# Optimization experiments

Hardware: AMD Instinct MI355X
Metric: run time of the kernel (lower is better)

The kernel has to match this reference:

```python
import jax, jax.numpy as jnp
import numpy as np

B, N, D_FEAT = 4, 2048, 3
P = B * N
C_KP, K_PTS, NSAMPLE = 64, 15, 64
RADIUS, WINDOW = 0.2, 0.25
KP_EXTENT = 0.08  # prev_grid_size * sigma
F, H, HID, L = 256, 8, 512, 2
DH = F // H
EPS = 1e-5


def setup_inputs() -> dict:
    key = jax.random.key(0)
    k = jax.random.split(key, 24)
    s = 0.02
    position = jax.random.uniform(k[0], (B, N, 3), jnp.float32)
    feature = jax.random.normal(k[1], (B, N, D_FEAT), jnp.float32)
    # KPConv kernel points: fixed points inside a ball of radius 1.5*KP_EXTENT
    d = jax.random.normal(k[2], (K_PTS, 3))
    d = d / jnp.clip(jnp.linalg.norm(d, axis=1, keepdims=True), 1e-6)
    r = jax.random.uniform(k[3], (K_PTS, 1)) ** (1.0 / 3.0)
    kernel_points = (d * r * 1.5 * KP_EXTENT).astype(jnp.float32)
    return dict(
        position=position,
        feature=feature,
        kernel_points=kernel_points,
        kp_weights=s * jax.random.normal(k[4], (K_PTS, D_FEAT, C_KP), jnp.float32),
        bn_gamma=jnp.ones((C_KP,), jnp.float32),
        bn_beta=jnp.zeros((C_KP,), jnp.float32),
        weightmatrix=jax.random.normal(k[5], (1, C_KP + 3, F), jnp.float32) * s,
        Wq=s * jax.random.normal(k[6], (L, F, F), jnp.float32),
        bq=jnp.zeros((L, F), jnp.float32),
        Wk=s * jax.random.normal(k[7], (L, F, F), jnp.float32),
        bk=jnp.zeros((L, F), jnp.float32),
        Wv=s * jax.random.normal(k[8], (L, F, F), jnp.float32),
        bv=jnp.zeros((L, F), jnp.float32),
        Wo=s * jax.random.normal(k[9], (L, F, F), jnp.float32),
        bo=jnp.zeros((L, F), jnp.float32),
        ln1_g=jnp.ones((L, F), jnp.float32),
        ln1_b=jnp.zeros((L, F), jnp.float32),
        W1=s * jax.random.normal(k[10], (L, F, HID), jnp.float32),
        b1=jnp.zeros((L, HID), jnp.float32),
        W2=s * jax.random.normal(k[11], (L, HID, F), jnp.float32),
        b2=jnp.zeros((L, F), jnp.float32),
        ln2_g=jnp.ones((L, F), jnp.float32),
        ln2_b=jnp.zeros((L, F), jnp.float32),
    )


def _ball_query(position):
    """partial_dense ball query: first NSAMPLE in-radius neighbors per point, fill=P."""
    def one(b, pb):
        d2 = jnp.sum((pb[:, None, :] - pb[None, :, :]) ** 2, -1)      # [N,N]
        within = d2 <= RADIUS ** 2
        # stable argsort puts in-radius indices first, in ascending index order
        order = jnp.argsort(jnp.where(within, 0, 1).astype(jnp.int32), axis=1)[:, :NSAMPLE]
        valid = jnp.arange(NSAMPLE)[None, :] < jnp.sum(within, axis=1)[:, None]
        return jnp.where(valid, order + b * N, P)
    return jax.vmap(one)(jnp.arange(B), position).reshape(P, NSAMPLE)


def _kpconv(pos_flat, feat_flat, idx, kernel_points, kp_weights, bn_gamma, bn_beta):
    pos_pad = jnp.concatenate([pos_flat, jnp.full((1, 3), 1e6, pos_flat.dtype)], 0)
    feat_pad = jnp.concatenate([feat_flat, jnp.zeros((1, feat_flat.shape[1]), feat_flat.dtype)], 0)
    neigh = pos_pad[idx] - pos_flat[:, None, :]                     # [P,NS,3]
    diff = neigh[:, :, None, :] - kernel_points[None, None]         # [P,NS,K,3]
    dist = jnp.sqrt(jnp.sum(diff * diff, -1) + 1e-12)               # [P,NS,K]
    infl = jnp.clip(1.0 - dist / KP_EXTENT, 0.0)                    # linear influence
    nf = feat_pad[idx]                                              # [P,NS,Din]
    wf = jnp.einsum('pnk,pnd->pkd', infl, nf)
    out = jnp.einsum('pkd,kdc->pc', wf, kp_weights)                 # [P,C]
    mu = out.mean(0)
    var = out.var(0)
    out = bn_gamma * (out - mu) * jax.lax.rsqrt(var + EPS) + bn_beta
    return jnp.where(out >= 0, out, 0.2 * out)                      # LeakyReLU(0.2)


def _cluster_mask(position):
    """grid_sample: same-voxel points attend to each other. Returns bool [B,N,N]."""
    start = position.min(axis=1, keepdims=True)
    cell = jnp.floor((position - start) / WINDOW).astype(jnp.int32)
    cid = cell[..., 0] * 4096 + cell[..., 1] * 64 + cell[..., 2]
    return cid[:, :, None] == cid[:, None, :]


def _ln(x, g, b):
    mu = x.mean(-1, keepdims=True)
    v = x.var(-1, keepdims=True)
    return g * (x - mu) * jax.lax.rsqrt(v + EPS) + b


def _enc(x, mask, Wq, bq, Wk, bk, Wv, bv, Wo, bo, g1, be1, W1, bb1, W2, bb2, g2, be2):
    q = (x @ Wq + bq).reshape(B, N, H, DH)
    k = (x @ Wk + bk).reshape(B, N, H, DH)
    v = (x @ Wv + bv).reshape(B, N, H, DH)
    s = jnp.einsum('bihd,bjhd->bhij', q, k) * (1.0 / np.sqrt(DH))
    s = jnp.where(mask[:, None, :, :], s, -1e9)
    p = jax.nn.softmax(s, -1)
    o = jnp.einsum('bhij,bjhd->bihd', p, v).reshape(B, N, F)
    x = _ln(x + o @ Wo + bo, g1, be1)
    h = jax.nn.relu(x @ W1 + bb1) @ W2 + bb2
    return _ln(x + h, g2, be2)


def reference(position, feature, kernel_points, kp_weights, bn_gamma, bn_beta, weightmatrix,
              Wq, bq, Wk, bk, Wv, bv, Wo, bo, ln1_g, ln1_b, W1, b1, W2, b2, ln2_g, ln2_b):
    pos_flat = position.reshape(P, 3)
    feat_flat = feature.reshape(P, D_FEAT)
    idx = _ball_query(position)
    kpf = _kpconv(pos_flat, feat_flat, idx, kernel_points, kp_weights, bn_gamma, bn_beta)
    kpf = kpf.reshape(B, N, C_KP)
    mask = _cluster_mask(position)
    pw = jnp.concatenate([position, kpf], -1)                       # [B,N,C+3]
    emb = jnp.einsum('bnc,cf->bnf', pw, weightmatrix[0])
    for l in range(L):
        emb = _enc(emb, mask, Wq[l], bq[l], Wk[l], bk[l], Wv[l], bv[l], Wo[l], bo[l],
                   ln1_g[l], ln1_b[l], W1[l], b1[l], W2[l], b2[l], ln2_g[l], ln2_b[l])
    return emb
```

## Files before the change

### kernel.cpp

```cpp
#include <hip/hip_runtime.h>
#include <math.h>

#define BATCH 4
#define NPTS  2048
#define PTS   8192
#define NS    64
#define KPTS  15
#define CKP   64
#define FDIM  256
#define HIDD  512
#define NHEAD 8
#define DHEAD 32
#define NLAY  2
#define R2    0.04f
#define KPE   0.08f
#define WIN   0.25f
#define EPSF  1e-5f
#define SCALE 0.17677669529663687f
#define CPITCH 264

typedef __attribute__((ext_vector_type(8))) short          short8;
typedef __attribute__((ext_vector_type(8))) unsigned short ushort8;
typedef __attribute__((ext_vector_type(4))) float          f32x4;

static __device__ __forceinline__ unsigned short f2bf(float f) {
    unsigned int u = __float_as_uint(f);
    unsigned int r = u + 0x7fffu + ((u >> 16) & 1u);
    return (unsigned short)(r >> 16);
}
static __device__ __forceinline__ float b2f(unsigned short u) {
    return __uint_as_float(((unsigned int)u) << 16);
}

__global__ __launch_bounds__(256) void prep_k(
    const float* __restrict__ pos,
    const float* __restrict__ Wq, const float* __restrict__ Wk,
    const float* __restrict__ Wv, const float* __restrict__ Wo,
    const float* __restrict__ W1, const float* __restrict__ W2,
    const float* __restrict__ bq, const float* __restrict__ bk,
    const float* __restrict__ bv,
    unsigned short* __restrict__ wT, float* __restrict__ bqkv,
    int* __restrict__ sorted, int* __restrict__ inv,
    int* __restrict__ offs, int* __restrict__ hist,
    unsigned long long* __restrict__ masks)
{
    __shared__ __align__(16) unsigned char sm[38400];
    int bid = blockIdx.x, tid = threadIdx.x;

    if (bid < 3072) {
        int z = bid >> 8, r = bid & 255;
        int bx = r & 15, by = r >> 4;
        int t = z >> 1, l = z & 1;
        const float* src; unsigned short* dst; int K, N;
        switch (t) {
            case 0: src=Wq+(size_t)l*65536;  dst=wT+(size_t)l*196608;           K=256; N=256; break;
            case 1: src=Wk+(size_t)l*65536;  dst=wT+(size_t)l*196608+65536;     K=256; N=256; break;
            case 2: src=Wv+(size_t)l*65536;  dst=wT+(size_t)l*196608+131072;    K=256; N=256; break;
            case 3: src=Wo+(size_t)l*65536;  dst=wT+393216+(size_t)l*65536;     K=256; N=256; break;
            case 4: src=W1+(size_t)l*131072; dst=wT+524288+(size_t)l*131072;    K=256; N=512; break;
            default:src=W2+(size_t)l*131072; dst=wT+786432+(size_t)l*131072;    K=512; N=256; break;
        }
        int n0 = bx*32, k0 = by*32;
        if (n0 >= N || k0 >= K) return;
        float* ld = (float*)sm;
        #pragma unroll
        for (int i = 0; i < 4; ++i) { int v=tid+i*256; int ty=v>>5, tx=v&31;
            ld[ty*33+tx] = src[(size_t)(k0+ty)*N + n0+tx]; }
        __syncthreads();
        #pragma unroll
        for (int i = 0; i < 4; ++i) { int v=tid+i*256; int ny=v>>5, nk=v&31;
            dst[(size_t)(n0+ny)*K + k0+nk] = f2bf(ld[nk*33+ny]); }
    } else if (bid < 3584) {
        int m_ = bid - 3072;
        int chunk = m_ & 31, b = (m_ >> 5) & 3, qg = m_ >> 7;
        int w = tid >> 6, lane = tid & 63;
        float* qx = (float*)sm; float* qy = qx + 512; float* qz = qy + 512;
        int qbase = qg * 512;
        for (int t = tid; t < 512; t += 256) {
            const float* q = pos + (size_t)(b*NPTS + qbase + t)*3;
            qx[t] = q[0]; qy[t] = q[1]; qz[t] = q[2];
        }
        const float* c = pos + (size_t)(b*NPTS + chunk*64 + lane)*3;
        float cx = c[0], cy = c[1], cz = c[2];
        __syncthreads();
        int q0 = w * 128;
        for (int i = 0; i < 128; ++i) {
            int qi = q0 + i;
            float dx = cx - qx[qi], dy = cy - qy[qi], dz = cz - qz[qi];
            float d2 = dx*dx + dy*dy + dz*dz;
            unsigned long long m = __ballot(d2 <= R2);
            if (lane == 0) masks[(size_t)(b*NPTS + qbase + qi)*32 + chunk] = m;
        }
    } else if (bid < 3588) {
        int b = bid - 3584;
        float* sx = (float*)sm; float* sy = sx + 256; float* sz = sy + 256;
        unsigned char* cid_s = sm + 3072;
        unsigned int* maskc = (unsigned int*)(sm + 5120);
        int* wpfx = (int*)(sm + 21504);
        int* tot  = (int*)(sm + 37888);
        int* off_c= (int*)(sm + 38144);
        float mx=1e30f, my=1e30f, mz=1e30f;
        for (int n = tid; n < NPTS; n += 256) {
            const float* q = pos + ((size_t)b*NPTS + n)*3;
            mx = fminf(mx, q[0]); my = fminf(my, q[1]); mz = fminf(mz, q[2]);
        }
        sx[tid]=mx; sy[tid]=my; sz[tid]=mz; __syncthreads();
        for (int o=128;o;o>>=1){ if(tid<o){sx[tid]=fminf(sx[tid],sx[tid+o]);sy[tid]=fminf(sy[tid],sy[tid+o]);sz[tid]=fminf(sz[tid],sz[tid+o]);} __syncthreads(); }
        float X = sx[0], Y = sy[0], Z = sz[0];
        __syncthreads();
        for (int i = tid; i < 64*64; i += 256) maskc[i] = 0u;
        __syncthreads();
        for (int n = tid; n < NPTS; n += 256) {
            const float* q = pos + ((size_t)b*NPTS + n)*3;
            int cx = (int)floorf((q[0]-X)/WIN);
            int cy = (int)floorf((q[1]-Y)/WIN);
            int cz = (int)floorf((q[2]-Z)/WIN);
            int c = (cx<<4) | (cy<<2) | cz;
            cid_s[n] = (unsigned char)c;
            atomicOr(&maskc[c*64 + (n>>5)], 1u << (n & 31));
        }
        __syncthreads();
        if (tid < 64) {
            int run = 0;
            for (int wd = 0; wd < 64; ++wd) { wpfx[tid*64+wd] = run; run += __popc(maskc[tid*64+wd]); }
            tot[tid] = run;
        }
        __syncthreads();
        if (tid == 0) { int run = 0; for (int c = 0; c < 64; ++c) { off_c[c] = run; run += tot[c]; } }
        __syncthreads();
        if (tid < 64) { hist[b*64+tid] = tot[tid]; offs[b*64+tid] = off_c[tid]; }
        for (int n = tid; n < NPTS; n += 256) {
            int c = cid_s[n];
            int wd = n >> 5;
            int rank = wpfx[c*64+wd] + __popc(maskc[c*64+wd] & ((1u << (n & 31)) - 1u));
            int slot = b*NPTS + off_c[c] + rank;
            int p = b*NPTS + n;
            sorted[slot] = p;
            inv[p] = slot;
        }
    } else {
        int i = (bid - 3588)*256 + tid;
        if (i < 2*768) {
            int l = i / 768, n = i - l*768;
            float v = (n < 256) ? bq[l*256+n] : (n < 512) ? bk[l*256+n-256] : bv[l*256+n-512];
            bqkv[l*768 + n] = v;
        }
    }
}

__global__ __launch_bounds__(256) void kpc_k(
    const float* __restrict__ pos, const float* __restrict__ feat,
    const unsigned long long* __restrict__ masks,
    const float* __restrict__ kpts, const float* __restrict__ kpw,
    float* __restrict__ raw)
{
    __shared__ int   idxs[64][66];
    __shared__ float kpwl[45*64];
    __shared__ float kpl[48];
    __shared__ float wfp[64*181 + 4];

    int tid = threadIdx.x, w = tid >> 6, lane = tid & 63;
    int pb = blockIdx.x * 64;
    int b = pb >> 11;
    int base = b * NPTS;

    for (int t = tid; t < 45*64; t += 256) kpwl[t] = kpw[t];
    if (tid < 45) kpl[tid] = kpts[tid];

    int g = tid >> 5, j = tid & 31;
    for (int pp = 0; pp < 8; ++pp) {
        int lp = pp*8 + g;
        unsigned long long m = masks[(size_t)(pb + lp)*32 + j];
        int cnt = __popcll(m);
        int inc = cnt;
        #pragma unroll
        for (int off = 1; off < 32; off <<= 1) {
            int v = __shfl_up(inc, off, 32);
            if (j >= off) inc += v;
        }
        int pfx = inc - cnt;
        int total = __shfl(inc, 31, 32);
        unsigned long long mm = m; int slot = pfx;
        while (mm && slot < NS) {
            int bit = __ffsll((long long)mm) - 1;
            idxs[lp][slot++] = j*64 + bit;
            mm &= mm - 1;
        }
        int cc = total < NS ? total : NS;
        for (int s = cc + j; s < NS; s += 32) idxs[lp][s] = NPTS;
    }
    __syncthreads();

    float wf[45];
    #pragma unroll
    for (int t = 0; t < 45; ++t) wf[t] = 0.f;
    {
        int p = pb + lane;
        float xi = pos[(size_t)p*3+0], yi = pos[(size_t)p*3+1], zi = pos[(size_t)p*3+2];
        for (int n = w*16; n < w*16 + 16; ++n) {
            int id = idxs[lane][n];
            if (id < NPTS) {
                const float* pq = pos + (size_t)(base + id)*3;
                float rx = pq[0]-xi, ry = pq[1]-yi, rz = pq[2]-zi;
                const float* ff = feat + (size_t)(base + id)*3;
                float g0 = ff[0], g1 = ff[1], g2 = ff[2];
                #pragma unroll
                for (int k = 0; k < KPTS; ++k) {
                    float dx = rx - kpl[k*3+0], dy = ry - kpl[k*3+1], dz = rz - kpl[k*3+2];
                    float dist = sqrtf(dx*dx + dy*dy + dz*dz + 1e-12f);
                    float infl = fmaxf(0.f, 1.0f - dist * (1.0f/KPE));
                    wf[k*3+0] = fmaf(infl, g0, wf[k*3+0]);
                    wf[k*3+1] = fmaf(infl, g1, wf[k*3+1]);
                    wf[k*3+2] = fmaf(infl, g2, wf[k*3+2]);
                }
            }
        }
    }
    #pragma unroll
    for (int t = 0; t < 45; ++t) wfp[lane*181 + t*4 + w] = wf[t];
    __syncthreads();
    for (int i = tid; i < 64*45; i += 256) {
        int p_ = i / 45, t = i - p_*45;
        float* q = &wfp[p_*181 + t*4];
        q[0] = (q[0]+q[1]) + (q[2]+q[3]);
    }
    __syncthreads();
    {
        int c = tid & 63, pg = tid >> 6;
        float kw[45];
        #pragma unroll
        for (int t = 0; t < 45; ++t) kw[t] = kpwl[t*64 + c];
        for (int p0 = 0; p0 < 16; p0 += 4) {
            float a0=0.f, a1=0.f, a2=0.f, a3=0.f;
            int pl = pg*16 + p0;
            #pragma unroll
            for (int t = 0; t < 45; ++t) {
                a0 = fmaf(kw[t], wfp[(pl+0)*181 + t*4], a0);
                a1 = fmaf(kw[t], wfp[(pl+1)*181 + t*4], a1);
                a2 = fmaf(kw[t], wfp[(pl+2)*181 + t*4], a2);
                a3 = fmaf(kw[t], wfp[(pl+3)*181 + t*4], a3);
            }
            raw[(size_t)(pb + pl+0)*CKP + c] = a0;
            raw[(size_t)(pb + pl+1)*CKP + c] = a1;
            raw[(size_t)(pb + pl+2)*CKP + c] = a2;
            raw[(size_t)(pb + pl+3)*CKP + c] = a3;
        }
    }
}

__global__ void bn_stats_k(const float* __restrict__ raw, float* __restrict__ stats)
{
    int c = blockIdx.x, tid = threadIdx.x;
    float s = 0.f, q = 0.f;
    for (int p = tid; p < PTS; p += 256) { float v = raw[p*CKP + c]; s += v; q += v*v; }
    __shared__ float sh[256], sh2[256];
    sh[tid]=s; sh2[tid]=q; __syncthreads();
    for (int o = 128; o; o >>= 1) { if (tid < o) { sh[tid]+=sh[tid+o]; sh2[tid]+=sh2[tid+o]; } __syncthreads(); }
    if (tid == 0) { stats[c] = sh[0]; stats[CKP + c] = sh2[0]; }
}

__global__ void embed_k(const float* __restrict__ pos, const float* __restrict__ raw,
                        const float* __restrict__ stats, const float* __restrict__ gamma,
                        const float* __restrict__ beta, const float* __restrict__ Wm,
                        const int* __restrict__ inv,
                        float* __restrict__ xs, unsigned short* __restrict__ xsb)
{
    int p = blockIdx.x, tid = threadIdx.x;
    __shared__ float pw[67];
    if (tid < 3) pw[tid] = pos[p*3 + tid];
    else if (tid < 67) {
        int c = tid - 3;
        float mu  = stats[c] * (1.0f/PTS);
        float var = stats[CKP+c] * (1.0f/PTS) - mu*mu;
        float v = raw[p*CKP + c];
        float h = gamma[c] * (v - mu) * rsqrtf(var + EPSF) + beta[c];
        pw[tid] = h >= 0.f ? h : 0.2f * h;
    }
    __syncthreads();
    float acc = 0.f;
    for (int c = 0; c < 67; ++c) acc += pw[c] * Wm[c*FDIM + tid];
    int slot = inv[p];
    xs[(size_t)slot*FDIM + tid] = acc;
    xsb[(size_t)slot*FDIM + tid] = f2bf(acc);
}

template<int ACT, int MR>
__global__ __launch_bounds__(256) void bgemm256_k(
    const unsigned short* __restrict__ A, const unsigned short* __restrict__ Wt,
    const float* __restrict__ bias,
    unsigned short* __restrict__ Cb,
    int Nc, int K)
{
    __shared__ unsigned short As[MR*16*72];
    __shared__ unsigned short Bs[256*72];
    int tid = threadIdx.x;
    int l = tid & 63, wc = tid >> 6;
    int lr = l & 15, lk = l >> 4;
    int bm = blockIdx.y * (MR*16), bn = blockIdx.x * 256;

    f32x4 acc[MR][4] = {};

    for (int k0 = 0; k0 < K; k0 += 64) {
        __syncthreads();
        #pragma unroll
        for (int i = 0; i < MR/2; ++i) {
            int id = tid + i*256;
            int row = id >> 3, seg = id & 7;
            *(ushort8*)&As[row*72 + seg*8] =
                *(const ushort8*)&A[(size_t)(bm + row)*K + k0 + seg*8];
        }
        #pragma unroll
        for (int i = 0; i < 8; ++i) {
            int id = tid + i*256;
            int row = id >> 3, seg = id & 7;
            *(ushort8*)&Bs[row*72 + seg*8] =
                *(const ushort8*)&Wt[(size_t)(bn + row)*K + k0 + seg*8];
        }
        __syncthreads();
        #pragma unroll
        for (int kk = 0; kk < 64; kk += 32) {
            short8 b[4];
            #pragma unroll
            for (int ni = 0; ni < 4; ++ni)
                b[ni] = *(const short8*)&Bs[(wc*64 + ni*16 + lr)*72 + kk + lk*8];
            #pragma unroll
            for (int mi = 0; mi < MR; ++mi) {
                short8 a = *(const short8*)&As[(mi*16 + lr)*72 + kk + lk*8];
                #pragma unroll
                for (int ni = 0; ni < 4; ++ni)
                    acc[mi][ni] = __builtin_amdgcn_mfma_f32_16x16x32_bf16(
                        a, b[ni], acc[mi][ni], 0, 0, 0);
            }
        }
    }

    #pragma unroll
    for (int mi = 0; mi < MR; ++mi) {
        #pragma unroll
        for (int r = 0; r < 4; ++r) {
            int row = bm + mi*16 + lk*4 + r;
            #pragma unroll
            for (int ni = 0; ni < 4; ++ni) {
                int col = bn + wc*64 + ni*16 + lr;
                float v = acc[mi][ni][r] + bias[col];
                if (ACT == 1) v = v > 0.f ? v : 0.f;
                Cb[(size_t)row*Nc + col] = f2bf(v);
            }
        }
    }
}

__global__ __launch_bounds__(512) void attn2_k(
    const unsigned short* __restrict__ qkv, const unsigned short* __restrict__ WoT,
    const float* __restrict__ bo, const float* __restrict__ xs,
    const float* __restrict__ g, const float* __restrict__ be,
    const int* __restrict__ offs, const int* __restrict__ hist,
    float* __restrict__ x2, unsigned short* __restrict__ x2b)
{
    int cci = blockIdx.x, b = blockIdx.y;
    int Mc = hist[b*64 + cci];
    if (Mc == 0) return;
    int off = b*NPTS + offs[b*64 + cci];

    __shared__ unsigned short Kl[64*CPITCH];
    __shared__ unsigned short Vl[64*CPITCH];
    __shared__ unsigned short Pl[8][64*72];

    unsigned short* Ol = Kl;
    unsigned short* Bs = &Pl[0][0];
    float* red_s = (float*)Vl;
    float* red_q = red_s + 512;

    int tid = threadIdx.x;
    int w = tid >> 6, l = tid & 63;
    int lr = l & 15, lk = l >> 4;

    for (int r0 = 0; r0 < Mc; r0 += 64) {
        int nr = (Mc - r0) < 64 ? (Mc - r0) : 64;

        if (Mc <= 64) {
            #pragma unroll
            for (int it = 0; it < 4; ++it) {
                int id = tid + it*512;
                int key = id >> 5, ch8 = (id & 31)*8;
                ushort8 kv, vv;
                if (key < Mc) {
                    kv = *(const ushort8*)&qkv[(size_t)(off+key)*768 + 256 + ch8];
                    vv = *(const ushort8*)&qkv[(size_t)(off+key)*768 + 512 + ch8];
                } else {
                    kv = (ushort8)0; vv = (ushort8)0;
                }
                *(ushort8*)&Kl[key*CPITCH + ch8] = kv;
                *(ushort8*)&Vl[key*CPITCH + ch8] = vv;
            }
            __syncthreads();

            int h = w;
            f32x4 s[4][4] = {};
            short8 a[4], bb[4];
            #pragma unroll
            for (int mi = 0; mi < 4; ++mi) {
                int rg = off + mi*16 + lr;
                if (rg > PTS-1) rg = PTS-1;
                a[mi] = *(const short8*)&qkv[(size_t)rg*768 + h*32 + lk*8];
            }
            #pragma unroll
            for (int ni = 0; ni < 4; ++ni)
                bb[ni] = *(const short8*)&Kl[(ni*16+lr)*CPITCH + h*32 + lk*8];
            #pragma unroll
            for (int mi = 0; mi < 4; ++mi)
                #pragma unroll
                for (int ni = 0; ni < 4; ++ni)
                    s[mi][ni] = __builtin_amdgcn_mfma_f32_16x16x32_bf16(a[mi], bb[ni], s[mi][ni], 0, 0, 0);

            unsigned short* Pw = Pl[w];
            float invl[4][4];
            #pragma unroll
            for (int mi = 0; mi < 4; ++mi) {
                #pragma unroll
                for (int r = 0; r < 4; ++r) {
                    int row = mi*16 + lk*4 + r;
                    float sv[4]; float mx = -1e30f;
                    #pragma unroll
                    for (int ni = 0; ni < 4; ++ni) {
                        int col = ni*16 + lr;
                        float x = s[mi][ni][r] * SCALE;
                        sv[ni] = (col < Mc) ? x : -1e30f;
                        mx = fmaxf(mx, sv[ni]);
                    }
                    mx = fmaxf(mx, __shfl_xor(mx, 1));
                    mx = fmaxf(mx, __shfl_xor(mx, 2));
                    mx = fmaxf(mx, __shfl_xor(mx, 4));
                    mx = fmaxf(mx, __shfl_xor(mx, 8));
                    float ls = 0.f;
                    #pragma unroll
                    for (int ni = 0; ni < 4; ++ni) {
                        float e = __expf(sv[ni] - mx);
                        ls += e;
                        Pw[row*72 + ni*16 + lr] = f2bf(e);
                    }
                    ls += __shfl_xor(ls, 1);
                    ls += __shfl_xor(ls, 2);
                    ls += __shfl_xor(ls, 4);
                    ls += __shfl_xor(ls, 8);
                    invl[mi][r] = 1.0f / ls;
                }
            }

            f32x4 oacc[4][2] = {};
            #pragma unroll
            for (int ks = 0; ks < 2; ++ks) {
                short8 bv[2];
                #pragma unroll
                for (int db = 0; db < 2; ++db) {
                    short8 t;
                    #pragma unroll
                    for (int e = 0; e < 8; ++e)
                        t[e] = (short)Vl[(ks*32 + lk*8 + e)*CPITCH + h*32 + db*16 + lr];
                    bv[db] = t;
                }
                #pragma unroll
                for (int mi = 0; mi < 4; ++mi) {
                    short8 pa = *(const short8*)&Pw[(mi*16+lr)*72 + ks*32 + lk*8];
                    #pragma unroll
                    for (int db = 0; db < 2; ++db)
                        oacc[mi][db] = __builtin_amdgcn_mfma_f32_16x16x32_bf16(pa, bv[db], oacc[mi][db], 0, 0, 0);
                }
            }
            __syncthreads();
            #pragma unroll
            for (int mi = 0; mi < 4; ++mi)
                #pragma unroll
                for (int db = 0; db < 2; ++db)
                    #pragma unroll
                    for (int r = 0; r < 4; ++r) {
                        int row = mi*16 + lk*4 + r;
                        Ol[row*CPITCH + h*32 + db*16 + lr] =
                            f2bf(oacc[mi][db][r] * invl[mi][r]);
                    }
        } else {
            __syncthreads();
            for (int task = tid; task < nr*NHEAD; task += 512) {
                int row = task >> 3, h = task & 7;
                float qr[DHEAD];
                #pragma unroll
                for (int d = 0; d < DHEAD; ++d)
                    qr[d] = b2f(qkv[(size_t)(off+r0+row)*768 + h*32 + d]);
                float m = -3e38f, lsum = 0.f, acc[DHEAD];
                #pragma unroll
                for (int d = 0; d < DHEAD; ++d) acc[d] = 0.f;
                for (int jj = 0; jj < Mc; ++jj) {
                    float dot = 0.f;
                    #pragma unroll
                    for (int d = 0; d < DHEAD; ++d)
                        dot += qr[d] * b2f(qkv[(size_t)(off+jj)*768 + 256 + h*32 + d]);
                    float sc = dot * SCALE;
                    float mn = fmaxf(m, sc);
                    float aa = __expf(m - mn);
                    float e  = __expf(sc - mn);
                    lsum = lsum*aa + e;
                    #pragma unroll
                    for (int d = 0; d < DHEAD; ++d)
                        acc[d] = acc[d]*aa + e * b2f(qkv[(size_t)(off+jj)*768 + 512 + h*32 + d]);
                    m = mn;
                }
                float inv = 1.0f / lsum;
                #pragma unroll
                for (int d = 0; d < DHEAD; ++d)
                    Ol[row*CPITCH + h*32 + d] = f2bf(acc[d]*inv);
            }
        }
        __syncthreads();

        f32x4 acc2[4][2] = {};
        for (int k0 = 0; k0 < 256; k0 += 64) {
            #pragma unroll
            for (int i = 0; i < 4; ++i) {
                int id = tid + i*512;
                int rown = id >> 3, seg = id & 7;
                *(ushort8*)&Bs[rown*72 + seg*8] =
                    *(const ushort8*)&WoT[(size_t)rown*FDIM + k0 + seg*8];
            }
            __syncthreads();
            #pragma unroll
            for (int kk = 0; kk < 64; kk += 32) {
                short8 a2[4], b2r[2];
                #pragma unroll
                for (int mi = 0; mi < 4; ++mi)
                    a2[mi] = *(const short8*)&Ol[(mi*16+lr)*CPITCH + k0 + kk + lk*8];
                #pragma unroll
                for (int ni = 0; ni < 2; ++ni)
                    b2r[ni] = *(const short8*)&Bs[(w*32 + ni*16 + lr)*72 + kk + lk*8];
                #pragma unroll
                for (int mi = 0; mi < 4; ++mi)
                    #pragma unroll
                    for (int ni = 0; ni < 2; ++ni)
                        acc2[mi][ni] = __builtin_amdgcn_mfma_f32_16x16x32_bf16(
                            a2[mi], b2r[ni], acc2[mi][ni], 0, 0, 0);
            }
            __syncthreads();
        }

        #pragma unroll
        for (int mi = 0; mi < 4; ++mi) {
            #pragma unroll
            for (int r = 0; r < 4; ++r) {
                int row = mi*16 + lk*4 + r;
                int srow = off + r0 + row;
                if (srow > PTS-1) srow = PTS-1;
                #pragma unroll
                for (int ni = 0; ni < 2; ++ni) {
                    int col = w*32 + ni*16 + lr;
                    acc2[mi][ni][r] += bo[col] + xs[(size_t)srow*FDIM + col];
                }
            }
        }
        #pragma unroll
        for (int mi = 0; mi < 4; ++mi) {
            #pragma unroll
            for (int r = 0; r < 4; ++r) {
                float ps = 0.f, pq = 0.f;
                #pragma unroll
                for (int ni = 0; ni < 2; ++ni) { float v = acc2[mi][ni][r]; ps += v; pq += v*v; }
                ps += __shfl_xor(ps, 1);  pq += __shfl_xor(pq, 1);
                ps += __shfl_xor(ps, 2);  pq += __shfl_xor(pq, 2);
                ps += __shfl_xor(ps, 4);  pq += __shfl_xor(pq, 4);
                ps += __shfl_xor(ps, 8);  pq += __shfl_xor(pq, 8);
                if (lr == 0) {
                    int row = mi*16 + lk*4 + r;
                    red_s[w*64 + row] = ps;
                    red_q[w*64 + row] = pq;
                }
            }
        }
        __syncthreads();
        #pragma unroll
        for (int mi = 0; mi < 4; ++mi) {
            #pragma unroll
            for (int r = 0; r < 4; ++r) {
                int row = mi*16 + lk*4 + r;
                float s = 0.f, q = 0.f;
                #pragma unroll
                for (int ww = 0; ww < 8; ++ww) { s += red_s[ww*64 + row]; q += red_q[ww*64 + row]; }
                float mu  = s * (1.0f/FDIM);
                float var = q * (1.0f/FDIM) - mu*mu;
                float rs  = rsqrtf(var + EPSF);
                if (row < nr) {
                    int srow = off + r0 + row;
                    #pragma unroll
                    for (int ni = 0; ni < 2; ++ni) {
                        int col = w*32 + ni*16 + lr;
                        float o = g[col]*(acc2[mi][ni][r]-mu)*rs + be[col];
                        x2[(size_t)srow*FDIM + col] = o;
                        x2b[(size_t)srow*FDIM + col] = f2bf(o);
                    }
                }
            }
        }
        __syncthreads();
    }
}

template<int FINAL>
__global__ __launch_bounds__(256) void ffn_k(
    const unsigned short* __restrict__ A,
    const unsigned short* __restrict__ W1T,
    const float* __restrict__ b1,
    const unsigned short* __restrict__ W2T,
    const float* __restrict__ b2,
    const float* __restrict__ R,
    const float* __restrict__ g, const float* __restrict__ be,
    const int* __restrict__ sorted,
    float* __restrict__ Cf, unsigned short* __restrict__ Cb)
{
    __shared__ unsigned short As[32*264];
    __shared__ unsigned short Bs1[64*264];
    __shared__ unsigned short Bs2[256*72];
    __shared__ unsigned short Hs[32*72];
    __shared__ float red_s[4][32], red_q[4][32];

    int tid = threadIdx.x;
    int l = tid & 63, wc = tid >> 6;
    int lr = l & 15, lk = l >> 4;
    int bm = blockIdx.x * 32;

    #pragma unroll
    for (int i = 0; i < 4; ++i) {
        int id = tid + i*256;
        int row = id >> 5, seg = id & 31;
        *(ushort8*)&As[row*264 + seg*8] =
            *(const ushort8*)&A[(size_t)(bm + row)*FDIM + seg*8];
    }

    f32x4 acc[2][4] = {};

    for (int hc = 0; hc < 8; ++hc) {
        __syncthreads();
        #pragma unroll
        for (int i = 0; i < 8; ++i) {
            int id = tid + i*256;
            int row = id >> 5, seg = id & 31;
            *(ushort8*)&Bs1[row*264 + seg*8] =
                *(const ushort8*)&W1T[(size_t)(hc*64 + row)*FDIM + seg*8];
        }
        #pragma unroll
        for (int i = 0; i < 8; ++i) {
            int id = tid + i*256;
            int row = id >> 3, seg = id & 7;
            *(ushort8*)&Bs2[row*72 + seg*8] =
                *(const ushort8*)&W2T[(size_t)row*HIDD + hc*64 + seg*8];
        }
        __syncthreads();

        f32x4 h[2] = {};
        #pragma unroll
        for (int kk = 0; kk < 256; kk += 32) {
            short8 bfr = *(const short8*)&Bs1[(wc*16 + lr)*264 + kk + lk*8];
            #pragma unroll
            for (int mi = 0; mi < 2; ++mi) {
                short8 a = *(const short8*)&As[(mi*16 + lr)*264 + kk + lk*8];
                h[mi] = __builtin_amdgcn_mfma_f32_16x16x32_bf16(a, bfr, h[mi], 0, 0, 0);
            }
        }
        #pragma unroll
        for (int mi = 0; mi < 2; ++mi)
            #pragma unroll
            for (int r = 0; r < 4; ++r) {
                int row = mi*16 + lk*4 + r;
                int hcol = wc*16 + lr;
                float v = h[mi][r] + b1[hc*64 + hcol];
                v = v > 0.f ? v : 0.f;
                Hs[row*72 + hcol] = f2bf(v);
            }
        __syncthreads();

        #pragma unroll
        for (int kk = 0; kk < 64; kk += 32) {
            short8 pa[2], wb[4];
            #pragma unroll
            for (int mi = 0; mi < 2; ++mi)
                pa[mi] = *(const short8*)&Hs[(mi*16 + lr)*72 + kk + lk*8];
            #pragma unroll
            for (int ni = 0; ni < 4; ++ni)
                wb[ni] = *(const short8*)&Bs2[(wc*64 + ni*16 + lr)*72 + kk + lk*8];
            #pragma unroll
            for (int mi = 0; mi < 2; ++mi)
                #pragma unroll
                for (int ni = 0; ni < 4; ++ni)
                    acc[mi][ni] = __builtin_amdgcn_mfma_f32_16x16x32_bf16(
                        pa[mi], wb[ni], acc[mi][ni], 0, 0, 0);
        }
    }

    #pragma unroll
    for (int mi = 0; mi < 2; ++mi) {
        #pragma unroll
        for (int r = 0; r < 4; ++r) {
            int row = bm + mi*16 + lk*4 + r;
            #pragma unroll
            for (int ni = 0; ni < 4; ++ni) {
                int col = wc*64 + ni*16 + lr;
                acc[mi][ni][r] += b2[col] + R[(size_t)row*FDIM + col];
            }
        }
    }
    #pragma unroll
    for (int mi = 0; mi < 2; ++mi) {
        #pragma unroll
        for (int r = 0; r < 4; ++r) {
            float ps = 0.f, pq = 0.f;
            #pragma unroll
            for (int ni = 0; ni < 4; ++ni) { float v = acc[mi][ni][r]; ps += v; pq += v*v; }
            ps += __shfl_xor(ps, 1);  pq += __shfl_xor(pq, 1);
            ps += __shfl_xor(ps, 2);  pq += __shfl_xor(pq, 2);
            ps += __shfl_xor(ps, 4);  pq += __shfl_xor(pq, 4);
            ps += __shfl_xor(ps, 8);  pq += __shfl_xor(pq, 8);
            if (lr == 0) {
                int rl = mi*16 + lk*4 + r;
                red_s[wc][rl] = ps;
                red_q[wc][rl] = pq;
            }
        }
    }
    __syncthreads();
    #pragma unroll
    for (int mi = 0; mi < 2; ++mi) {
        #pragma unroll
        for (int r = 0; r < 4; ++r) {
            int rl = mi*16 + lk*4 + r;
            float s = red_s[0][rl] + red_s[1][rl] + red_s[2][rl] + red_s[3][rl];
            float q = red_q[0][rl] + red_q[1][rl] + red_q[2][rl] + red_q[3][rl];
            float mu  = s * (1.0f/FDIM);
            float var = q * (1.0f/FDIM) - mu*mu;
            float rs  = rsqrtf(var + EPSF);
            int row = bm + rl;
            #pragma unroll
            for (int ni = 0; ni < 4; ++ni) {
                int col = wc*64 + ni*16 + lr;
                float o = g[col]*(acc[mi][ni][r]-mu)*rs + be[col];
                if (FINAL) Cf[(size_t)sorted[row]*FDIM + col] = o;
                else       Cf[(size_t)row*FDIM + col] = o;
                if (Cb) Cb[(size_t)row*FDIM + col] = f2bf(o);
            }
        }
    }
}

extern "C" void kernel_launch(void* const* d_in, const int* in_sizes, int n_in,
                              void* d_out, int out_size, void* d_ws, size_t ws_size,
                              hipStream_t stream)
{
    (void)in_sizes; (void)n_in; (void)out_size; (void)ws_size;
    const float* pos  = (const float*)d_in[0];
    const float* feat = (const float*)d_in[1];
    const float* kpts = (const float*)d_in[2];
    const float* kpw  = (const float*)d_in[3];
    const float* bn_g = (const float*)d_in[4];
    const float* bn_b = (const float*)d_in[5];
    const float* Wm   = (const float*)d_in[6];
    const float* Wq   = (const float*)d_in[7];
    const float* bq   = (const float*)d_in[8];
    const float* Wk   = (const float*)d_in[9];
    const float* bk   = (const float*)d_in[10];
    const float* Wv   = (const float*)d_in[11];
    const float* bv   = (const float*)d_in[12];
    const float* Wo   = (const float*)d_in[13];
    const float* bo   = (const float*)d_in[14];
    const float* g1   = (const float*)d_in[15];
    const float* be1  = (const float*)d_in[16];
    const float* W1   = (const float*)d_in[17];
    const float* bb1  = (const float*)d_in[18];
    const float* W2   = (const float*)d_in[19];
    const float* bb2  = (const float*)d_in[20];
    const float* g2   = (const float*)d_in[21];
    const float* be2  = (const float*)d_in[22];

    char* ws = (char*)d_ws;
    const size_t MB = 1024*1024;
    float* raw    = (float*)(ws + 0);
    unsigned long long* masks = (unsigned long long*)(ws + 2*MB);
    float* stats  = (float*)(ws + 4*MB);
    int*   hist   = (int*)(ws + 4*MB + 4096);
    int*   offs   = hist + 256;
    int*   sorted = (int*)(ws + 4*MB + 16384);
    int*   inv    = sorted + PTS;
    float* xs   = (float*)(ws + 5*MB);
    float* x2   = (float*)(ws + 13*MB);
    unsigned short* xsb   = (unsigned short*)(ws + 21*MB);
    unsigned short* x2b   = (unsigned short*)(ws + 25*MB);
    unsigned short* qkvb  = (unsigned short*)(ws + 29*MB);
    unsigned short* wT    = (unsigned short*)(ws + 45*MB);
    float*          bqkv  = (float*)(ws + 47*MB);

    prep_k<<<3594, 256, 0, stream>>>(pos, Wq, Wk, Wv, Wo, W1, W2, bq, bk, bv,
                                     wT, bqkv, sorted, inv, offs, hist, masks);
    kpc_k<<<PTS/64, 256, 0, stream>>>(pos, feat, masks, kpts, kpw, raw);
    bn_stats_k<<<CKP, 256, 0, stream>>>(raw, stats);
    embed_k<<<PTS, 256, 0, stream>>>(pos, raw, stats, bn_g, bn_b, Wm, inv, xs, xsb);

    for (int l = 0; l < NLAY; ++l) {
        const unsigned short* W1T_l = wT + 524288 + (size_t)l*131072;
        const unsigned short* W2T_l = wT + 786432 + (size_t)l*131072;
        bgemm256_k<0,8><<<dim3(3, PTS/128), 256, 0, stream>>>(
            xsb, wT + (size_t)l*196608, bqkv + l*768, qkvb, 768, FDIM);
        attn2_k<<<dim3(64, BATCH), 512, 0, stream>>>(
            qkvb, wT + 393216 + (size_t)l*65536, bo + l*FDIM, xs,
            g1 + l*FDIM, be1 + l*FDIM, offs, hist, x2, x2b);
        if (l == NLAY-1)
            ffn_k<1><<<PTS/32, 256, 0, stream>>>(
                x2b, W1T_l, bb1 + l*HIDD, W2T_l, bb2 + l*FDIM, x2,
                g2 + l*FDIM, be2 + l*FDIM, sorted, (float*)d_out, nullptr);
        else
            ffn_k<0><<<PTS/32, 256, 0, stream>>>(
                x2b, W1T_l, bb1 + l*HIDD, W2T_l, bb2 + l*FDIM, x2,
                g2 + l*FDIM, be2 + l*FDIM, nullptr, xs, xsb);
    }
}
```

Before: 215.2 us.

## Fuse per-layer QKV GEMM, attention and FFN into one cooperative persistent kernel

Replaces the three per-layer launches (QKV GEMM, attention+Wo+LN, FFN+LN) across two layers with a single cooperative kernel of 256 blocks that steps through the stages with grid-wide syncs. The aim is to remove launch overhead and inter-kernel gaps. In exchange the grid is limited to 256 blocks of 512 threads with about 138 KB of LDS each, which gives low occupancy for the GEMM and FFN phases. Grid syncs and thread fences also add cost.

```diff
diff --git a/kernel.cpp b/kernel.cpp
--- a/kernel.cpp
+++ b/kernel.cpp
@@ -1,5 +1,8 @@
 #include <hip/hip_runtime.h>
+#include <hip/hip_cooperative_groups.h>
 #include <math.h>
+
+namespace cg = cooperative_groups;
 
 #define BATCH 4
 #define NPTS  2048
@@ -284,466 +287,484 @@
     xsb[(size_t)slot*FDIM + tid] = f2bf(acc);
 }
 
-template<int ACT, int MR>
-__global__ __launch_bounds__(256) void bgemm256_k(
-    const unsigned short* __restrict__ A, const unsigned short* __restrict__ Wt,
-    const float* __restrict__ bias,
-    unsigned short* __restrict__ Cb,
-    int Nc, int K)
+__global__ __launch_bounds__(512) void mega_k(
+    const unsigned short* __restrict__ xsb_in, float* __restrict__ xs,
+    unsigned short* __restrict__ xsb,
+    const unsigned short* __restrict__ wT, const float* __restrict__ bqkv,
+    const float* __restrict__ bo, const float* __restrict__ g1,
+    const float* __restrict__ be1, const float* __restrict__ bb1,
+    const float* __restrict__ bb2, const float* __restrict__ g2,
+    const float* __restrict__ be2,
+    const int* __restrict__ offs, const int* __restrict__ hist,
+    const int* __restrict__ sorted,
+    unsigned short* __restrict__ qkvb, float* __restrict__ x2,
+    unsigned short* __restrict__ x2b, float* __restrict__ dout)
 {
-    __shared__ unsigned short As[MR*16*72];
-    __shared__ unsigned short Bs[256*72];
-    int tid = threadIdx.x;
-    int l = tid & 63, wc = tid >> 6;
-    int lr = l & 15, lk = l >> 4;
-    int bm = blockIdx.y * (MR*16), bn = blockIdx.x * 256;
-
-    f32x4 acc[MR][4] = {};
-
-    for (int k0 = 0; k0 < K; k0 += 64) {
-        __syncthreads();
-        #pragma unroll
-        for (int i = 0; i < MR/2; ++i) {
-            int id = tid + i*256;
-            int row = id >> 3, seg = id & 7;
-            *(ushort8*)&As[row*72 + seg*8] =
-                *(const ushort8*)&A[(size_t)(bm + row)*K + k0 + seg*8];
-        }
-        #pragma unroll
-        for (int i = 0; i < 8; ++i) {
-            int id = tid + i*256;
-            int row = id >> 3, seg = id & 7;
-            *(ushort8*)&Bs[row*72 + seg*8] =
-                *(const ushort8*)&Wt[(size_t)(bn + row)*K + k0 + seg*8];
-        }
-        __syncthreads();
-        #pragma unroll
-        for (int kk = 0; kk < 64; kk += 32) {
-            short8 b[4];
+    __shared__ __align__(16) unsigned char smem[141312];
+    cg::grid_group grid = cg::this_grid();
+
+    int bid = blockIdx.x, tid = threadIdx.x;
+    int w = tid >> 6, l_ = tid & 63;
+    int lr = l_ & 15, lk = l_ >> 4;
+
+    for (int l = 0; l < NLAY; ++l) {
+        const unsigned short* WqkvT = wT + (size_t)l*196608;
+        const unsigned short* WoT   = wT + 393216 + (size_t)l*65536;
+        const unsigned short* W1T   = wT + 524288 + (size_t)l*131072;
+        const unsigned short* W2T   = wT + 786432 + (size_t)l*131072;
+        const float* bqkv_l = bqkv + l*768;
+        const float* bo_l   = bo  + l*FDIM;
+        const float* g1_l   = g1  + l*FDIM;
+        const float* be1_l  = be1 + l*FDIM;
+        const float* b1_l   = bb1 + l*HIDD;
+        const float* b2_l   = bb2 + l*FDIM;
+        const float* g2_l   = g2  + l*FDIM;
+        const float* be2_l  = be2 + l*FDIM;
+
+        if (bid < 192) {
+            unsigned short* As = (unsigned short*)smem;
+            unsigned short* Bs = As + 128*72;
+            int bm = (bid / 3) * 128, bn = (bid % 3) * 256;
+            int wr = w >> 2, wc4 = w & 3;
+            f32x4 acc[4][4] = {};
+            for (int k0 = 0; k0 < FDIM; k0 += 64) {
+                __syncthreads();
+                #pragma unroll
+                for (int i = 0; i < 2; ++i) {
+                    int id = tid + i*512;
+                    int row = id >> 3, seg = id & 7;
+                    *(ushort8*)&As[row*72 + seg*8] =
+                        *(const ushort8*)&xsb[(size_t)(bm + row)*FDIM + k0 + seg*8];
+                }
+                #pragma unroll
+                for (int i = 0; i < 4; ++i) {
+                    int id = tid + i*512;
+                    int row = id >> 3, seg = id & 7;
+                    *(ushort8*)&Bs[row*72 + seg*8] =
+                        *(const ushort8*)&WqkvT[(size_t)(bn + row)*FDIM + k0 + seg*8];
+                }
+                __syncthreads();
+                #pragma unroll
+                for (int kk = 0; kk < 64; kk += 32) {
+                    short8 bb[4];
+                    #pragma unroll
+                    for (int ni = 0; ni < 4; ++ni)
+                        bb[ni] = *(const short8*)&Bs[(wc4*64 + ni*16 + lr)*72 + kk + lk*8];
+                    #pragma unroll
+                    for (int mi = 0; mi < 4; ++mi) {
+                        short8 a = *(const short8*)&As[(wr*64 + mi*16 + lr)*72 + kk + lk*8];
+                        #pragma unroll
+                        for (int ni = 0; ni < 4; ++ni)
+                            acc[mi][ni] = __builtin_amdgcn_mfma_f32_16x16x32_bf16(
+                                a, bb[ni], acc[mi][ni], 0, 0, 0);
+                    }
+                }
+            }
             #pragma unroll
-            for (int ni = 0; ni < 4; ++ni)
-                b[ni] = *(const short8*)&Bs[(wc*64 + ni*16 + lr)*72 + kk + lk*8];
+            for (int mi = 0; mi < 4; ++mi)
+                #pragma unroll
+                for (int r = 0; r < 4; ++r) {
+                    int row = bm + wr*64 + mi*16 + lk*4 + r;
+                    #pragma unroll
+                    for (int ni = 0; ni < 4; ++ni) {
+                        int col = bn + wc4*64 + ni*16 + lr;
+                        qkvb[(size_t)row*768 + col] = f2bf(acc[mi][ni][r] + bqkv_l[col]);
+                    }
+                }
+        }
+        __threadfence();
+        grid.sync();
+
+        {
+            int cci = bid & 63, bb_ = bid >> 6;
+            int Mc = hist[bb_*64 + cci];
+            if (Mc != 0) {
+                int off = bb_*NPTS + offs[bb_*64 + cci];
+                unsigned short* Kl = (unsigned short*)smem;
+                unsigned short* Vl = Kl + 64*CPITCH;
+                unsigned short* Pl = Vl + 64*CPITCH;
+                unsigned short* Ol = Kl;
+                unsigned short* Bs = Pl;
+                float* red_s = (float*)Vl;
+                float* red_q = red_s + 512;
+
+                for (int r0 = 0; r0 < Mc; r0 += 64) {
+                    int nr = (Mc - r0) < 64 ? (Mc - r0) : 64;
+
+                    if (Mc <= 64) {
+                        #pragma unroll
+                        for (int it = 0; it < 4; ++it) {
+                            int id = tid + it*512;
+                            int key = id >> 5, ch8 = (id & 31)*8;
+                            ushort8 kv, vv;
+                            if (key < Mc) {
+                                kv = *(const ushort8*)&qkvb[(size_t)(off+key)*768 + 256 + ch8];
+                                vv = *(const ushort8*)&qkvb[(size_t)(off+key)*768 + 512 + ch8];
+                            } else {
+                                kv = (ushort8)0; vv = (ushort8)0;
+                            }
+                            *(ushort8*)&Kl[key*CPITCH + ch8] = kv;
+                            *(ushort8*)&Vl[key*CPITCH + ch8] = vv;
+                        }
+                        __syncthreads();
+
+                        int h = w;
+                        f32x4 s[4][4] = {};
+                        short8 a[4], bb[4];
+                        #pragma unroll
+                        for (int mi = 0; mi < 4; ++mi) {
+                            int rg = off + mi*16 + lr;
+                            if (rg > PTS-1) rg = PTS-1;
+                            a[mi] = *(const short8*)&qkvb[(size_t)rg*768 + h*32 + lk*8];
+                        }
+                        #pragma unroll
+                        for (int ni = 0; ni < 4; ++ni)
+                            bb[ni] = *(const short8*)&Kl[(ni*16+lr)*CPITCH + h*32 + lk*8];
+                        #pragma unroll
+                        for (int mi = 0; mi < 4; ++mi)
+                            #pragma unroll
+                            for (int ni = 0; ni < 4; ++ni)
+                                s[mi][ni] = __builtin_amdgcn_mfma_f32_16x16x32_bf16(a[mi], bb[ni], s[mi][ni], 0, 0, 0);
+
+                        unsigned short* Pw = Pl + w*4608;
+                        float invl[4][4];
+                        #pragma unroll
+                        for (int mi = 0; mi < 4; ++mi) {
+                            #pragma unroll
+                            for (int r = 0; r < 4; ++r) {
+                                int row = mi*16 + lk*4 + r;
+                                float sv[4]; float mx = -1e30f;
+                                #pragma unroll
+                                for (int ni = 0; ni < 4; ++ni) {
+                                    int col = ni*16 + lr;
+                                    float x = s[mi][ni][r] * SCALE;
+                                    sv[ni] = (col < Mc) ? x : -1e30f;
+                                    mx = fmaxf(mx, sv[ni]);
+                                }
+                                mx = fmaxf(mx, __shfl_xor(mx, 1));
+                                mx = fmaxf(mx, __shfl_xor(mx, 2));
+                                mx = fmaxf(mx, __shfl_xor(mx, 4));
+                                mx = fmaxf(mx, __shfl_xor(mx, 8));
+                                float ls = 0.f;
+                                #pragma unroll
+                                for (int ni = 0; ni < 4; ++ni) {
+                                    float e = __expf(sv[ni] - mx);
+                                    ls += e;
+                                    Pw[row*72 + ni*16 + lr] = f2bf(e);
+                                }
+                                ls += __shfl_xor(ls, 1);
+                                ls += __shfl_xor(ls, 2);
+                                ls += __shfl_xor(ls, 4);
+                                ls += __shfl_xor(ls, 8);
+                                invl[mi][r] = 1.0f / ls;
+                            }
+                        }
+
+                        f32x4 oacc[4][2] = {};
+                        #pragma unroll
+                        for (int ks = 0; ks < 2; ++ks) {
+                            short8 bv[2];
+                            #pragma unroll
+                            for (int db = 0; db < 2; ++db) {
+                                short8 t;
+                                #pragma unroll
+                                for (int e = 0; e < 8; ++e)
+                                    t[e] = (short)Vl[(ks*32 + lk*8 + e)*CPITCH + h*32 + db*16 + lr];
+                                bv[db] = t;
+                            }
+                            #pragma unroll
+                            for (int mi = 0; mi < 4; ++mi) {
+                                short8 pa = *(const short8*)&Pw[(mi*16+lr)*72 + ks*32 + lk*8];
+                                #pragma unroll
+                                for (int db = 0; db < 2; ++db)
+                                    oacc[mi][db] = __builtin_amdgcn_mfma_f32_16x16x32_bf16(pa, bv[db], oacc[mi][db], 0, 0, 0);
+                            }
+                        }
+                        __syncthreads();
+                        #pragma unroll
+                        for (int mi = 0; mi < 4; ++mi)
+                            #pragma unroll
+                            for (int db = 0; db < 2; ++db)
+                                #pragma unroll
+                                for (int r = 0; r < 4; ++r) {
+                                    int row = mi*16 + lk*4 + r;
+                                    Ol[row*CPITCH + h*32 + db*16 + lr] =
+                                        f2bf(oacc[mi][db][r] * invl[mi][r]);
+                                }
+                    } else {
+                        __syncthreads();
+                        for (int task = tid; task < nr*NHEAD; task += 512) {
+                            int row = task >> 3, h = task & 7;
+                            float qr[DHEAD];
+                            #pragma unroll
+                            for (int d = 0; d < DHEAD; ++d)
+                                qr[d] = b2f(qkvb[(size_t)(off+r0+row)*768 + h*32 + d]);
+                            float m = -3e38f, lsum = 0.f, acc[DHEAD];
+                            #pragma unroll
+                            for (int d = 0; d < DHEAD; ++d) acc[d] = 0.f;
+                            for (int jj = 0; jj < Mc; ++jj) {
+                                float dot = 0.f;
+                                #pragma unroll
+                                for (int d = 0; d < DHEAD; ++d)
+                                    dot += qr[d] * b2f(qkvb[(size_t)(off+jj)*768 + 256 + h*32 + d]);
+                                float sc = dot * SCALE;
+                                float mn = fmaxf(m, sc);
+                                float aa = __expf(m - mn);
+                                float e  = __expf(sc - mn);
+                                lsum = lsum*aa + e;
+                                #pragma unroll
+                                for (int d = 0; d < DHEAD; ++d)
+                                    acc[d] = acc[d]*aa + e * b2f(qkvb[(size_t)(off+jj)*768 + 512 + h*32 + d]);
+                                m = mn;
+                            }
+                            float inv = 1.0f / lsum;
+                            #pragma unroll
+                            for (int d = 0; d < DHEAD; ++d)
+                                Ol[row*CPITCH + h*32 + d] = f2bf(acc[d]*inv);
+                        }
+                    }
+                    __syncthreads();
+
+                    f32x4 acc2[4][2] = {};
+                    for (int k0 = 0; k0 < 256; k0 += 64) {
+                        #pragma unroll
+                        for (int i = 0; i < 4; ++i) {
+                            int id = tid + i*512;
+                            int rown = id >> 3, seg = id & 7;
+                            *(ushort8*)&Bs[rown*72 + seg*8] =
+                                *(const ushort8*)&WoT[(size_t)rown*FDIM + k0 + seg*8];
+                        }
+                        __syncthreads();
+                        #pragma unroll
+                        for (int kk = 0; kk < 64; kk += 32) {
+                            short8 a2[4], b2r[2];
+                            #pragma unroll
+                            for (int mi = 0; mi < 4; ++mi)
+                                a2[mi] = *(const short8*)&Ol[(mi*16+lr)*CPITCH + k0 + kk + lk*8];
+                            #pragma unroll
+                            for (int ni = 0; ni < 2; ++ni)
+                                b2r[ni] = *(const short8*)&Bs[(w*32 + ni*16 + lr)*72 + kk + lk*8];
+                            #pragma unroll
+                            for (int mi = 0; mi < 4; ++mi)
+                                #pragma unroll
+                                for (int ni = 0; ni < 2; ++ni)
+                                    acc2[mi][ni] = __builtin_amdgcn_mfma_f32_16x16x32_bf16(
+                                        a2[mi], b2r[ni], acc2[mi][ni], 0, 0, 0);
+                        }
+                        __syncthreads();
+                    }
+
+                    #pragma unroll
+                    for (int mi = 0; mi < 4; ++mi) {
+                        #pragma unroll
+                        for (int r = 0; r < 4; ++r) {
+                            int row = mi*16 + lk*4 + r;
+                            int srow = off + r0 + row;
+                            if (srow > PTS-1) srow = PTS-1;
+                            #pragma unroll
+                            for (int ni = 0; ni < 2; ++ni) {
+                                int col = w*32 + ni*16 + lr;
+                                acc2[mi][ni][r] += bo_l[col] + xs[(size_t)srow*FDIM + col];
+                            }
+                        }
+                    }
+                    #pragma unroll
+                    for (int mi = 0; mi < 4; ++mi) {
+                        #pragma unroll
+                        for (int r = 0; r < 4; ++r) {
+                            float ps = 0.f, pq = 0.f;
+                            #pragma unroll
+                            for (int ni = 0; ni < 2; ++ni) { float v = acc2[mi][ni][r]; ps += v; pq += v*v; }
+                            ps += __shfl_xor(ps, 1);  pq += __shfl_xor(pq, 1);
+                            ps += __shfl_xor(ps, 2);  pq += __shfl_xor(pq, 2);
+                            ps += __shfl_xor(ps, 4);  pq += __shfl_xor(pq, 4);
+                            ps += __shfl_xor(ps, 8);  pq += __shfl_xor(pq, 8);
+                            if (lr == 0) {
+                                int row = mi*16 + lk*4 + r;
+                                red_s[w*64 + row] = ps;
+                                red_q[w*64 + row] = pq;
+                            }
+                        }
+                    }
+                    __syncthreads();
+                    #pragma unroll
+                    for (int mi = 0; mi < 4; ++mi) {
+                        #pragma unroll
+                        for (int r = 0; r < 4; ++r) {
+                            int row = mi*16 + lk*4 + r;
+                            float s_ = 0.f, q_ = 0.f;
+                            #pragma unroll
+                            for (int ww = 0; ww < 8; ++ww) { s_ += red_s[ww*64 + row]; q_ += red_q[ww*64 + row]; }
+                            float mu  = s_ * (1.0f/FDIM);
+                            float var = q_ * (1.0f/FDIM) - mu*mu;
+                            float rs  = rsqrtf(var + EPSF);
+                            if (row < nr) {
+                                int srow = off + r0 + row;
+                                #pragma unroll
+                                for (int ni = 0; ni < 2; ++ni) {
+                                    int col = w*32 + ni*16 + lr;
+                                    float o = g1_l[col]*(acc2[mi][ni][r]-mu)*rs + be1_l[col];
+                                    x2[(size_t)srow*FDIM + col] = o;
+                                    x2b[(size_t)srow*FDIM + col] = f2bf(o);
+                                }
+                            }
+                        }
+                    }
+                    __syncthreads();
+                }
+            }
+        }
+        __threadfence();
+        grid.sync();
+
+        {
+            unsigned short* As  = (unsigned short*)smem;
+            unsigned short* Bs1 = As + 32*264;
+            unsigned short* Bs2 = Bs1 + 64*264;
+            unsigned short* Hs  = Bs2 + 256*72;
+            float* red_s = (float*)(Hs + 32*72);
+            float* red_q = red_s + 128;
+            int bm = bid * 32;
+            int wc = w;
+
             #pragma unroll
-            for (int mi = 0; mi < MR; ++mi) {
-                short8 a = *(const short8*)&As[(mi*16 + lr)*72 + kk + lk*8];
-                #pragma unroll
-                for (int ni = 0; ni < 4; ++ni)
-                    acc[mi][ni] = __builtin_amdgcn_mfma_f32_16x16x32_bf16(
-                        a, b[ni], acc[mi][ni], 0, 0, 0);
+            for (int i = 0; i < 2; ++i) {
+                int id = tid + i*512;
+                int row = id >> 5, seg = id & 31;
+                *(ushort8*)&As[row*264 + seg*8] =
+                    *(const ushort8*)&x2b[(size_t)(bm + row)*FDIM + seg*8];
             }
-        }
-    }
-
-    #pragma unroll
-    for (int mi = 0; mi < MR; ++mi) {
-        #pragma unroll
-        for (int r = 0; r < 4; ++r) {
-            int row = bm + mi*16 + lk*4 + r;
-            #pragma unroll
-            for (int ni = 0; ni < 4; ++ni) {
-                int col = bn + wc*64 + ni*16 + lr;
-                float v = acc[mi][ni][r] + bias[col];
-                if (ACT == 1) v = v > 0.f ? v : 0.f;
-                Cb[(size_t)row*Nc + col] = f2bf(v);
+
+            f32x4 acc[2][4] = {};
+
+            for (int hc = 0; hc < 8; ++hc) {
+                __syncthreads();
+                #pragma unroll
+                for (int i = 0; i < 4; ++i) {
+                    int id = tid + i*512;
+                    int row = id >> 5, seg = id & 31;
+                    *(ushort8*)&Bs1[row*264 + seg*8] =
+                        *(const ushort8*)&W1T[(size_t)(hc*64 + row)*FDIM + seg*8];
+                }
+                #pragma unroll
+                for (int i = 0; i < 4; ++i) {
+                    int id = tid + i*512;
+                    int row = id >> 3, seg = id & 7;
+                    *(ushort8*)&Bs2[row*72 + seg*8] =
+                        *(const ushort8*)&W2T[(size_t)row*HIDD + hc*64 + seg*8];
+                }
+                __syncthreads();
+
+                if (tid < 256) {
+                    f32x4 h[2] = {};
+                    #pragma unroll
+                    for (int kk = 0; kk < 256; kk += 32) {
+                        short8 bfr = *(const short8*)&Bs1[(wc*16 + lr)*264 + kk + lk*8];
+                        #pragma unroll
+                        for (int mi = 0; mi < 2; ++mi) {
+                            short8 a = *(const short8*)&As[(mi*16 + lr)*264 + kk + lk*8];
+                            h[mi] = __builtin_amdgcn_mfma_f32_16x16x32_bf16(a, bfr, h[mi], 0, 0, 0);
+                        }
+                    }
+                    #pragma unroll
+                    for (int mi = 0; mi < 2; ++mi)
+                        #pragma unroll
+                        for (int r = 0; r < 4; ++r) {
+                            int row = mi*16 + lk*4 + r;
+                            int hcol = wc*16 + lr;
+                            float v = h[mi][r] + b1_l[hc*64 + hcol];
+                            v = v > 0.f ? v : 0.f;
+                            Hs[row*72 + hcol] = f2bf(v);
+                        }
+                }
+                __syncthreads();
+
+                if (tid < 256) {
+                    #pragma unroll
+                    for (int kk = 0; kk < 64; kk += 32) {
+                        short8 pa[2], wb[4];
+                        #pragma unroll
+                        for (int mi = 0; mi < 2; ++mi)
+                            pa[mi] = *(const short8*)&Hs[(mi*16 + lr)*72 + kk + lk*8];
+                        #pragma unroll
+                        for (int ni = 0; ni < 4; ++ni)
+                            wb[ni] = *(const short8*)&Bs2[(wc*64 + ni*16 + lr)*72 + kk + lk*8];
+                        #pragma unroll
+                        for (int mi = 0; mi < 2; ++mi)
+                            #pragma unroll
+                            for (int ni = 0; ni < 4; ++ni)
+                                acc[mi][ni] = __builtin_amdgcn_mfma_f32_16x16x32_bf16(
+                                    pa[mi], wb[ni], acc[mi][ni], 0, 0, 0);
+                    }
+                }
             }
-        }
-    }
-}
-
-__global__ __launch_bounds__(512) void attn2_k(
-    const unsigned short* __restrict__ qkv, const unsigned short* __restrict__ WoT,
-    const float* __restrict__ bo, const float* __restrict__ xs,
-    const float* __restrict__ g, const float* __restrict__ be,
-    const int* __restrict__ offs, const int* __restrict__ hist,
-    float* __restrict__ x2, unsigned short* __restrict__ x2b)
-{
-    int cci = blockIdx.x, b = blockIdx.y;
-    int Mc = hist[b*64 + cci];
-    if (Mc == 0) return;
-    int off = b*NPTS + offs[b*64 + cci];
-
-    __shared__ unsigned short Kl[64*CPITCH];
-    __shared__ unsigned short Vl[64*CPITCH];
-    __shared__ unsigned short Pl[8][64*72];
-
-    unsigned short* Ol = Kl;
-    unsigned short* Bs = &Pl[0][0];
-    float* red_s = (float*)Vl;
-    float* red_q = red_s + 512;
-
-    int tid = threadIdx.x;
-    int w = tid >> 6, l = tid & 63;
-    int lr = l & 15, lk = l >> 4;
-
-    for (int r0 = 0; r0 < Mc; r0 += 64) {
-        int nr = (Mc - r0) < 64 ? (Mc - r0) : 64;
-
-        if (Mc <= 64) {
-            #pragma unroll
-            for (int it = 0; it < 4; ++it) {
-                int id = tid + it*512;
-                int key = id >> 5, ch8 = (id & 31)*8;
-                ushort8 kv, vv;
-                if (key < Mc) {
-                    kv = *(const ushort8*)&qkv[(size_t)(off+key)*768 + 256 + ch8];
-                    vv = *(const ushort8*)&qkv[(size_t)(off+key)*768 + 512 + ch8];
-                } else {
-                    kv = (ushort8)0; vv = (ushort8)0;
-                }
-                *(ushort8*)&Kl[key*CPITCH + ch8] = kv;
-                *(ushort8*)&Vl[key*CPITCH + ch8] = vv;
+
+            if (tid < 256) {
+                #pragma unroll
+                for (int mi = 0; mi < 2; ++mi) {
+                    #pragma unroll
+                    for (int r = 0; r < 4; ++r) {
+                        int row = bm + mi*16 + lk*4 + r;
+                        #pragma unroll
+                        for (int ni = 0; ni < 4; ++ni) {
+                            int col = wc*64 + ni*16 + lr;
+                            acc[mi][ni][r] += b2_l[col] + x2[(size_t)row*FDIM + col];
+                        }
+                    }
+                }
+                #pragma unroll
+                for (int mi = 0; mi < 2; ++mi) {
+                    #pragma unroll
+                    for (int r = 0; r < 4; ++r) {
+                        float ps = 0.f, pq = 0.f;
+                        #pragma unroll
+                        for (int ni = 0; ni < 4; ++ni) { float v = acc[mi][ni][r]; ps += v; pq += v*v; }
+                        ps += __shfl_xor(ps, 1);  pq += __shfl_xor(pq, 1);
+                        ps += __shfl_xor(ps, 2);  pq += __shfl_xor(pq, 2);
+                        ps += __shfl_xor(ps, 4);  pq += __shfl_xor(pq, 4);
+                        ps += __shfl_xor(ps, 8);  pq += __shfl_xor(pq, 8);
+                        if (lr == 0) {
+                            int rl = mi*16 + lk*4 + r;
+                            red_s[wc*32 + rl] = ps;
+                            red_q[wc*32 + rl] = pq;
+                        }
+                    }
+                }
             }
             __syncthreads();
-
-            int h = w;
-            f32x4 s[4][4] = {};
-            short8 a[4], bb[4];
-            #pragma unroll
-            for (int mi = 0; mi < 4; ++mi) {
-                int rg = off + mi*16 + lr;
-                if (rg > PTS-1) rg = PTS-1;
-                a[mi] = *(const short8*)&qkv[(size_t)rg*768 + h*32 + lk*8];
+            if (tid < 256) {
+                #pragma unroll
+                for (int mi = 0; mi < 2; ++mi) {
+                    #pragma unroll
+                    for (int r = 0; r < 4; ++r) {
+                        int rl = mi*16 + lk*4 + r;
+                        float s = red_s[0*32+rl] + red_s[1*32+rl] + red_s[2*32+rl] + red_s[3*32+rl];
+                        float q = red_q[0*32+rl] + red_q[1*32+rl] + red_q[2*32+rl] + red_q[3*32+rl];
+                        float mu  = s * (1.0f/FDIM);
+                        float var = q * (1.0f/FDIM) - mu*mu;
+                        float rs  = rsqrtf(var + EPSF);
+                        int row = bm + rl;
+                        #pragma unroll
+                        for (int ni = 0; ni < 4; ++ni) {
+                            int col = wc*64 + ni*16 + lr;
+                            float o = g2_l[col]*(acc[mi][ni][r]-mu)*rs + be2_l[col];
+                            if (l == NLAY-1) {
+                                dout[(size_t)sorted[row]*FDIM + col] = o;
+                            } else {
+                                xs[(size_t)row*FDIM + col] = o;
+                                xsb[(size_t)row*FDIM + col] = f2bf(o);
+                            }
+                        }
+                    }
+                }
             }
-            #pragma unroll
-            for (int ni = 0; ni < 4; ++ni)
-                bb[ni] = *(const short8*)&Kl[(ni*16+lr)*CPITCH + h*32 + lk*8];
-            #pragma unroll
-            for (int mi = 0; mi < 4; ++mi)
-                #pragma unroll
-                for (int ni = 0; ni < 4; ++ni)
-                    s[mi][ni] = __builtin_amdgcn_mfma_f32_16x16x32_bf16(a[mi], bb[ni], s[mi][ni], 0, 0, 0);
-
-            unsigned short* Pw = Pl[w];
-            float invl[4][4];
-            #pragma unroll
-            for (int mi = 0; mi < 4; ++mi) {
-                #pragma unroll
-                for (int r = 0; r < 4; ++r) {
-                    int row = mi*16 + lk*4 + r;
-                    float sv[4]; float mx = -1e30f;
-                    #pragma unroll
-                    for (int ni = 0; ni < 4; ++ni) {
-                        int col = ni*16 + lr;
-                        float x = s[mi][ni][r] * SCALE;
-                        sv[ni] = (col < Mc) ? x : -1e30f;
-                        mx = fmaxf(mx, sv[ni]);
-                    }
-                    mx = fmaxf(mx, __shfl_xor(mx, 1));
-                    mx = fmaxf(mx, __shfl_xor(mx, 2));
-                    mx = fmaxf(mx, __shfl_xor(mx, 4));
-                    mx = fmaxf(mx, __shfl_xor(mx, 8));
-                    float ls = 0.f;
-                    #pragma unroll
-                    for (int ni = 0; ni < 4; ++ni) {
-                        float e = __expf(sv[ni] - mx);
-                        ls += e;
-                        Pw[row*72 + ni*16 + lr] = f2bf(e);
-                    }
-                    ls += __shfl_xor(ls, 1);
-                    ls += __shfl_xor(ls, 2);
-                    ls += __shfl_xor(ls, 4);
-                    ls += __shfl_xor(ls, 8);
-                    invl[mi][r] = 1.0f / ls;
-                }
-            }
-
-            f32x4 oacc[4][2] = {};
-            #pragma unroll
-            for (int ks = 0; ks < 2; ++ks) {
-                short8 bv[2];
-                #pragma unroll
-                for (int db = 0; db < 2; ++db) {
-                    short8 t;
-                    #pragma unroll
-                    for (int e = 0; e < 8; ++e)
-                        t[e] = (short)Vl[(ks*32 + lk*8 + e)*CPITCH + h*32 + db*16 + lr];
-                    bv[db] = t;
-                }
-                #pragma unroll
-                for (int mi = 0; mi < 4; ++mi) {
-                    short8 pa = *(const short8*)&Pw[(mi*16+lr)*72 + ks*32 + lk*8];
-                    #pragma unroll
-                    for (int db = 0; db < 2; ++db)
-                        oacc[mi][db] = __builtin_amdgcn_mfma_f32_16x16x32_bf16(pa, bv[db], oacc[mi][db], 0, 0, 0);
-                }
-            }
-            __syncthreads();
-            #pragma unroll
-            for (int mi = 0; mi < 4; ++mi)
-                #pragma unroll
-                for (int db = 0; db < 2; ++db)
-                    #pragma unroll
-                    for (int r = 0; r < 4; ++r) {
-                        int row = mi*16 + lk*4 + r;
-                        Ol[row*CPITCH + h*32 + db*16 + lr] =
-                            f2bf(oacc[mi][db][r] * invl[mi][r]);
-                    }
-        } else {
-            __syncthreads();
-            for (int task = tid; task < nr*NHEAD; task += 512) {
-                int row = task >> 3, h = task & 7;
-                float qr[DHEAD];
-                #pragma unroll
-                for (int d = 0; d < DHEAD; ++d)
-                    qr[d] = b2f(qkv[(size_t)(off+r0+row)*768 + h*32 + d]);
-                float m = -3e38f, lsum = 0.f, acc[DHEAD];
-                #pragma unroll
-                for (int d = 0; d < DHEAD; ++d) acc[d] = 0.f;
-                for (int jj = 0; jj < Mc; ++jj) {
-                    float dot = 0.f;
-                    #pragma unroll
-                    for (int d = 0; d < DHEAD; ++d)
-                        dot += qr[d] * b2f(qkv[(size_t)(off+jj)*768 + 256 + h*32 + d]);
-                    float sc = dot * SCALE;
-                    float mn = fmaxf(m, sc);
-                    float aa = __expf(m - mn);
-                    float e  = __expf(sc - mn);
-                    lsum = lsum*aa + e;
-                    #pragma unroll
-                    for (int d = 0; d < DHEAD; ++d)
-                        acc[d] = acc[d]*aa + e * b2f(qkv[(size_t)(off+jj)*768 + 512 + h*32 + d]);
-                    m = mn;
-                }
-                float inv = 1.0f / lsum;
-                #pragma unroll
-                for (int d = 0; d < DHEAD; ++d)
-                    Ol[row*CPITCH + h*32 + d] = f2bf(acc[d]*inv);
-            }
-        }
-        __syncthreads();
-
-        f32x4 acc2[4][2] = {};
-        for (int k0 = 0; k0 < 256; k0 += 64) {
-            #pragma unroll
-            for (int i = 0; i < 4; ++i) {
-                int id = tid + i*512;
-                int rown = id >> 3, seg = id & 7;
-                *(ushort8*)&Bs[rown*72 + seg*8] =
-                    *(const ushort8*)&WoT[(size_t)rown*FDIM + k0 + seg*8];
-            }
-            __syncthreads();
-            #pragma unroll
-            for (int kk = 0; kk < 64; kk += 32) {
-                short8 a2[4], b2r[2];
-                #pragma unroll
-                for (int mi = 0; mi < 4; ++mi)
-                    a2[mi] = *(const short8*)&Ol[(mi*16+lr)*CPITCH + k0 + kk + lk*8];
-                #pragma unroll
-                for (int ni = 0; ni < 2; ++ni)
-                    b2r[ni] = *(const short8*)&Bs[(w*32 + ni*16 + lr)*72 + kk + lk*8];
-                #pragma unroll
-                for (int mi = 0; mi < 4; ++mi)
-                    #pragma unroll
-                    for (int ni = 0; ni < 2; ++ni)
-                        acc2[mi][ni] = __builtin_amdgcn_mfma_f32_16x16x32_bf16(
-                            a2[mi], b2r[ni], acc2[mi][ni], 0, 0, 0);
-            }
-            __syncthreads();
-        }
-
-        #pragma unroll
-        for (int mi = 0; mi < 4; ++mi) {
-            #pragma unroll
-            for (int r = 0; r < 4; ++r) {
-                int row = mi*16 + lk*4 + r;
-                int srow = off + r0 + row;
-                if (srow > PTS-1) srow = PTS-1;
-                #pragma unroll
-                for (int ni = 0; ni < 2; ++ni) {
-                    int col = w*32 + ni*16 + lr;
-                    acc2[mi][ni][r] += bo[col] + xs[(size_t)srow*FDIM + col];
-                }
-            }
-        }
-        #pragma unroll
-        for (int mi = 0; mi < 4; ++mi) {
-            #pragma unroll
-            for (int r = 0; r < 4; ++r) {
-                float ps = 0.f, pq = 0.f;
-                #pragma unroll
-                for (int ni = 0; ni < 2; ++ni) { float v = acc2[mi][ni][r]; ps += v; pq += v*v; }
-                ps += __shfl_xor(ps, 1);  pq += __shfl_xor(pq, 1);
-                ps += __shfl_xor(ps, 2);  pq += __shfl_xor(pq, 2);
-                ps += __shfl_xor(ps, 4);  pq += __shfl_xor(pq, 4);
-                ps += __shfl_xor(ps, 8);  pq += __shfl_xor(pq, 8);
-                if (lr == 0) {
-                    int row = mi*16 + lk*4 + r;
-                    red_s[w*64 + row] = ps;
-                    red_q[w*64 + row] = pq;
-                }
-            }
-        }
-        __syncthreads();
-        #pragma unroll
-        for (int mi = 0; mi < 4; ++mi) {
-            #pragma unroll
-            for (int r = 0; r < 4; ++r) {
-                int row = mi*16 + lk*4 + r;
-                float s = 0.f, q = 0.f;
-                #pragma unroll
-                for (int ww = 0; ww < 8; ++ww) { s += red_s[ww*64 + row]; q += red_q[ww*64 + row]; }
-                float mu  = s * (1.0f/FDIM);
-                float var = q * (1.0f/FDIM) - mu*mu;
-                float rs  = rsqrtf(var + EPSF);
-                if (row < nr) {
-                    int srow = off + r0 + row;
-                    #pragma unroll
-                    for (int ni = 0; ni < 2; ++ni) {
-                        int col = w*32 + ni*16 + lr;
-                        float o = g[col]*(acc2[mi][ni][r]-mu)*rs + be[col];
-                        x2[(size_t)srow*FDIM + col] = o;
-                        x2b[(size_t)srow*FDIM + col] = f2bf(o);
-                    }
-                }
-            }
-        }
-        __syncthreads();
+        }
+        if (l < NLAY-1) {
+            __threadfence();
+            grid.sync();
+        }
     }
-}
-
-template<int FINAL>
-__global__ __launch_bounds__(256) void ffn_k(
-    const unsigned short* __restrict__ A,
-    const unsigned short* __restrict__ W1T,
-    const float* __restrict__ b1,
-    const unsigned short* __restrict__ W2T,
-    const float* __restrict__ b2,
-    const float* __restrict__ R,
-    const float* __restrict__ g, const float* __restrict__ be,
-    const int* __restrict__ sorted,
-    float* __restrict__ Cf, unsigned short* __restrict__ Cb)
-{
-    __shared__ unsigned short As[32*264];
-    __shared__ unsigned short Bs1[64*264];
-    __shared__ unsigned short Bs2[256*72];
-    __shared__ unsigned short Hs[32*72];
-    __shared__ float red_s[4][32], red_q[4][32];
-
-    int tid = threadIdx.x;
-    int l = tid & 63, wc = tid >> 6;
-    int lr = l & 15, lk = l >> 4;
-    int bm = blockIdx.x * 32;
-
-    #pragma unroll
-    for (int i = 0; i < 4; ++i) {
-        int id = tid + i*256;
-        int row = id >> 5, seg = id & 31;
-        *(ushort8*)&As[row*264 + seg*8] =
-            *(const ushort8*)&A[(size_t)(bm + row)*FDIM + seg*8];
-    }
-
-    f32x4 acc[2][4] = {};
-
-    for (int hc = 0; hc < 8; ++hc) {
-        __syncthreads();
-        #pragma unroll
-        for (int i = 0; i < 8; ++i) {
-            int id = tid + i*256;
-            int row = id >> 5, seg = id & 31;
-            *(ushort8*)&Bs1[row*264 + seg*8] =
-                *(const ushort8*)&W1T[(size_t)(hc*64 + row)*FDIM + seg*8];
-        }
-        #pragma unroll
-        for (int i = 0; i < 8; ++i) {
-            int id = tid + i*256;
-            int row = id >> 3, seg = id & 7;
-            *(ushort8*)&Bs2[row*72 + seg*8] =
-                *(const ushort8*)&W2T[(size_t)row*HIDD + hc*64 + seg*8];
-        }
-        __syncthreads();
-
-        f32x4 h[2] = {};
-        #pragma unroll
-        for (int kk = 0; kk < 256; kk += 32) {
-            short8 bfr = *(const short8*)&Bs1[(wc*16 + lr)*264 + kk + lk*8];
-            #pragma unroll
-            for (int mi = 0; mi < 2; ++mi) {
-                short8 a = *(const short8*)&As[(mi*16 + lr)*264 + kk + lk*8];
-                h[mi] = __builtin_amdgcn_mfma_f32_16x16x32_bf16(a, bfr, h[mi], 0, 0, 0);
-            }
-        }
-        #pragma unroll
-        for (int mi = 0; mi < 2; ++mi)
-            #pragma unroll
-            for (int r = 0; r < 4; ++r) {
-                int row = mi*16 + lk*4 + r;
-                int hcol = wc*16 + lr;
-                float v = h[mi][r] + b1[hc*64 + hcol];
-                v = v > 0.f ? v : 0.f;
-                Hs[row*72 + hcol] = f2bf(v);
-            }
-        __syncthreads();
-
-        #pragma unroll
-        for (int kk = 0; kk < 64; kk += 32) {
-            short8 pa[2], wb[4];
-            #pragma unroll
-            for (int mi = 0; mi < 2; ++mi)
-                pa[mi] = *(const short8*)&Hs[(mi*16 + lr)*72 + kk + lk*8];
-            #pragma unroll
-            for (int ni = 0; ni < 4; ++ni)
-                wb[ni] = *(const short8*)&Bs2[(wc*64 + ni*16 + lr)*72 + kk + lk*8];
-            #pragma unroll
-            for (int mi = 0; mi < 2; ++mi)
-                #pragma unroll
-                for (int ni = 0; ni < 4; ++ni)
-                    acc[mi][ni] = __builtin_amdgcn_mfma_f32_16x16x32_bf16(
-                        pa[mi], wb[ni], acc[mi][ni], 0, 0, 0);
-        }
-    }
-
-    #pragma unroll
-    for (int mi = 0; mi < 2; ++mi) {
-        #pragma unroll
-        for (int r = 0; r < 4; ++r) {
-            int row = bm + mi*16 + lk*4 + r;
-            #pragma unroll
-            for (int ni = 0; ni < 4; ++ni) {
-                int col = wc*64 + ni*16 + lr;
-                acc[mi][ni][r] += b2[col] + R[(size_t)row*FDIM + col];
-            }
-        }
-    }
-    #pragma unroll
-    for (int mi = 0; mi < 2; ++mi) {
-        #pragma unroll
-        for (int r = 0; r < 4; ++r) {
-            float ps = 0.f, pq = 0.f;
-            #pragma unroll
-            for (int ni = 0; ni < 4; ++ni) { float v = acc[mi][ni][r]; ps += v; pq += v*v; }
-            ps += __shfl_xor(ps, 1);  pq += __shfl_xor(pq, 1);
-            ps += __shfl_xor(ps, 2);  pq += __shfl_xor(pq, 2);
-            ps += __shfl_xor(ps, 4);  pq += __shfl_xor(pq, 4);
-            ps += __shfl_xor(ps, 8);  pq += __shfl_xor(pq, 8);
-            if (lr == 0) {
-                int rl = mi*16 + lk*4 + r;
-                red_s[wc][rl] = ps;
-                red_q[wc][rl] = pq;
-            }
-        }
-    }
-    __syncthreads();
-    #pragma unroll
-    for (int mi = 0; mi < 2; ++mi) {
-        #pragma unroll
-        for (int r = 0; r < 4; ++r) {
-            int rl = mi*16 + lk*4 + r;
-            float s = red_s[0][rl] + red_s[1][rl] + red_s[2][rl] + red_s[3][rl];
-            float q = red_q[0][rl] + red_q[1][rl] + red_q[2][rl] + red_q[3][rl];
-            float mu  = s * (1.0f/FDIM);
-            float var = q * (1.0f/FDIM) - mu*mu;
-            float rs  = rsqrtf(var + EPSF);
-            int row = bm + rl;
-            #pragma unroll
-            for (int ni = 0; ni < 4; ++ni) {
-                int col = wc*64 + ni*16 + lr;
-                float o = g[col]*(acc[mi][ni][r]-mu)*rs + be[col];
-                if (FINAL) Cf[(size_t)sorted[row]*FDIM + col] = o;
-                else       Cf[(size_t)row*FDIM + col] = o;
-                if (Cb) Cb[(size_t)row*FDIM + col] = f2bf(o);
-            }
-        }
-    }
+    (void)xsb_in;
 }
 
 extern "C" void kernel_launch(void* const* d_in, const int* in_sizes, int n_in,
@@ -798,21 +819,15 @@
     bn_stats_k<<<CKP, 256, 0, stream>>>(raw, stats);
     embed_k<<<PTS, 256, 0, stream>>>(pos, raw, stats, bn_g, bn_b, Wm, inv, xs, xsb);
 
-    for (int l = 0; l < NLAY; ++l) {
-        const unsigned short* W1T_l = wT + 524288 + (size_t)l*131072;
-        const unsigned short* W2T_l = wT + 786432 + (size_t)l*131072;
-        bgemm256_k<0,8><<<dim3(3, PTS/128), 256, 0, stream>>>(
-            xsb, wT + (size_t)l*196608, bqkv + l*768, qkvb, 768, FDIM);
-        attn2_k<<<dim3(64, BATCH), 512, 0, stream>>>(
-            qkvb, wT + 393216 + (size_t)l*65536, bo + l*FDIM, xs,
-            g1 + l*FDIM, be1 + l*FDIM, offs, hist, x2, x2b);
-        if (l == NLAY-1)
-            ffn_k<1><<<PTS/32, 256, 0, stream>>>(
-                x2b, W1T_l, bb1 + l*HIDD, W2T_l, bb2 + l*FDIM, x2,
-                g2 + l*FDIM, be2 + l*FDIM, sorted, (float*)d_out, nullptr);
-        else
-            ffn_k<0><<<PTS/32, 256, 0, stream>>>(
-                x2b, W1T_l, bb1 + l*HIDD, W2T_l, bb2 + l*FDIM, x2,
-                g2 + l*FDIM, be2 + l*FDIM, nullptr, xs, xsb);
+    {
+        const unsigned short* xsb_in = xsb;
+        float* dout = (float*)d_out;
+        void* ka[] = {
+            (void*)&xsb_in, (void*)&xs, (void*)&xsb, (void*)&wT, (void*)&bqkv,
+            (void*)&bo, (void*)&g1, (void*)&be1, (void*)&bb1, (void*)&bb2,
+            (void*)&g2, (void*)&be2, (void*)&offs, (void*)&hist, (void*)&sorted,
+            (void*)&qkvb, (void*)&x2, (void*)&x2b, (void*)&dout
+        };
+        hipLaunchCooperativeKernel((void*)mega_k, dim3(256), dim3(512), ka, 0, stream);
     }
 }
```

Result: slower. 770.7 us (+258.1%).
